# Kernel optimization log

Measured on AMD Instinct MI355X. Metric: run time of the kernel, lower is better.

## Reference

```python
import jax, jax.numpy as jnp
import numpy as np

DIM = 64
HID = 64      # hidden_dim
BATCH = 16384


def setup_inputs() -> dict:
    key = jax.random.key(0)
    ks = jax.random.split(key, 11)
    s = 0.05
    x = jax.random.normal(ks[0], (BATCH, DIM), dtype=jnp.float32)
    # network 0: Linear(1,H) -> ReLU -> Linear(H,2)
    w0 = jax.random.normal(ks[1], (1, HID), dtype=jnp.float32) * s
    b0 = jax.random.normal(ks[2], (HID,), dtype=jnp.float32) * s
    v0 = jax.random.normal(ks[3], (HID, 2), dtype=jnp.float32) * s
    c0 = jax.random.normal(ks[4], (2,), dtype=jnp.float32) * s
    # networks 1..DIM-1: Linear(i,H) -> ReLU -> Linear(H,H) -> ReLU -> Linear(H,2)
    # first-layer weights padded to full width DIM; columns >= i are masked out in reference().
    W1 = jax.random.normal(ks[5], (DIM - 1, DIM, HID), dtype=jnp.float32) * s
    B1 = jax.random.normal(ks[6], (DIM - 1, HID), dtype=jnp.float32) * s
    W2 = jax.random.normal(ks[7], (DIM - 1, HID, HID), dtype=jnp.float32) * s
    B2 = jax.random.normal(ks[8], (DIM - 1, HID), dtype=jnp.float32) * s
    W3 = jax.random.normal(ks[9], (DIM - 1, HID, 2), dtype=jnp.float32) * s
    B3 = jax.random.normal(ks[10], (DIM - 1, 2), dtype=jnp.float32) * s
    return {"x": x, "w0": w0, "b0": b0, "v0": v0, "c0": c0,
            "W1": W1, "B1": B1, "W2": W2, "B2": B2, "W3": W3, "B3": B3}


def reference(x, w0, b0, v0, c0, W1, B1, W2, B2, W3, B3):
    B, dim = x.shape
    # mask[i, j] = 1 if j < (i+1): network i+1 sees x[:, :i+1] prefix of width i+1... actually width i+1? No:
    # network index k (k = 1..dim-1) sees x[:, :k]. Row i of the stacks corresponds to k = i+1,
    # so valid input columns are j < i+1.
    mask = (jnp.arange(dim)[None, :] <= jnpp_dummy) if False else (jnp.arange(dim)[None, :] < (jnp.arange(1, dim)[:, None]))
    mask = mask.astype(x.dtype)                      # [dim-1, dim]
    W1m = W1 * mask[:, :, None]                      # zero out padded input columns
    h1 = jax.nn.relu(jnp.einsum('bd,idh->bih', x, W1m) + B1)   # [B, dim-1, H]
    h2 = jax.nn.relu(jnp.einsum('bih,ihg->big', h1, W2) + B2)  # [B, dim-1, H]
    out = jnp.einsum('big,igo->bio', h2, W3) + B3               # [B, dim-1, 2]
    # network 0 receives a constant ones input -> output is constant across the batch
    h0 = jax.nn.relu(w0[0] + b0)                     # [H]
    out0 = h0 @ v0 + c0                              # [2]
    out0 = jnp.broadcast_to(out0[None, None, :], (B, 1, 2))
    full = jnp.concatenate([out0, out], axis=1)      # [B, dim, 2]
    scales = jnp.clip(full[..., 0], -5.0, 5.0)
    translations = full[..., 1]
    return scales, translations

jnp_dummy = None
```

## Files before the change

### kernel.cpp

```cpp
#include <hip/hip_runtime.h>
#include <hip/hip_bf16.h>

#define BATCH 16384

typedef __attribute__((ext_vector_type(8))) short short8;
typedef __attribute__((ext_vector_type(4))) short short4v;
typedef __attribute__((ext_vector_type(2))) short sshort2;
typedef __attribute__((ext_vector_type(8))) unsigned short ushort8;
typedef __attribute__((ext_vector_type(4))) unsigned short ushort4v;
typedef __attribute__((ext_vector_type(4))) float float4v;

#define FR_A1      0u
#define FR_A2      516096u
#define FR_A3      1032192u
#define FR_SIZE    1161216u
#define XBF_SIZE   2097152u

__device__ __forceinline__ unsigned int packbf2(float a, float b) {
#if __has_builtin(__builtin_amdgcn_cvt_pk_bf16_f32)
    typedef __attribute__((ext_vector_type(2))) __bf16 bf2_t;
    union { bf2_t h; unsigned int u; } v;
    v.h = __builtin_amdgcn_cvt_pk_bf16_f32(a, b);
    return v.u;
#else
    union { __hip_bfloat162 h; unsigned int u; } v;
    v.h = __float22bfloat162_rn(make_float2(a, b));
    return v.u;
#endif
}
__device__ __forceinline__ unsigned int relu_pk(unsigned int u) {
#if __has_builtin(__builtin_elementwise_max)
    union { sshort2 s; unsigned int w; } v; v.w = u;
    v.s = __builtin_elementwise_max(v.s, (sshort2)0);
    return v.w;
#else
    unsigned int lo = (u & 0x8000u) ? 0u : (u & 0xFFFFu);
    unsigned int hi = (u & 0x80000000u) ? 0u : (u & 0xFFFF0000u);
    return lo | hi;
#endif
}
__device__ __forceinline__ unsigned int cvt_relu(float a, float b) {
    return relu_pk(packbf2(a, b));
}
__device__ __forceinline__ unsigned short f2bf(float a) {
    union { __hip_bfloat16 h; unsigned short u; } v;
    v.h = __float2bfloat16(a);
    return v.u;
}

__global__ __launch_bounds__(256) void setup_kernel(
    const float* __restrict__ x,
    const float* __restrict__ W1,
    const float* __restrict__ W2,
    const float* __restrict__ W3,
    char* __restrict__ frag,
    char* __restrict__ xbf)
{
    const int b = blockIdx.x;
    const int t = threadIdx.x;

    if (b >= 63) {
        const int idx = (b - 63) * 256 + t;
        const float* xp = x + (size_t)idx * 16;
        char* dst = xbf + (size_t)idx * 32;
        #pragma unroll
        for (int h = 0; h < 2; ++h) {
            float4v f0 = *(const float4v*)(xp + h * 8);
            float4v f1 = *(const float4v*)(xp + h * 8 + 4);
            union { ushort8 s; unsigned int u[4]; } p;
            p.u[0] = packbf2(f0[0], f0[1]);
            p.u[1] = packbf2(f0[2], f0[3]);
            p.u[2] = packbf2(f1[0], f1[1]);
            p.u[3] = packbf2(f1[2], f1[3]);
            *(ushort8*)(dst + h * 16) = p.s;
        }
        return;
    }

    const int kn   = b;
    const int net  = kn + 1;
    const int lane = t & 63;
    const int grp  = t >> 6;
    const int lq   = lane & 15;
    const int quad = lane >> 4;

    {
        const int h = lq + 16 * grp;
        ushort8 a10, a11;
        #pragma unroll
        for (int j = 0; j < 8; ++j) {
            const int d0 = quad * 8 + j;
            const int d1 = d0 + 32;
            a10[j] = (d0 < net) ? f2bf(W1[kn * 4096 + d0 * 64 + h]) : (unsigned short)0;
            a11[j] = (d1 < net) ? f2bf(W1[kn * 4096 + d1 * 64 + h]) : (unsigned short)0;
        }
        char* dst = frag + FR_A1 + kn * 8192 + grp * 2048 + lane * 32;
        *(ushort8*)(dst)      = a10;
        *(ushort8*)(dst + 16) = a11;
    }

    {
        const int g = lq + 16 * grp;
        #pragma unroll
        for (int th = 0; th < 4; ++th) {
            ushort4v v;
            #pragma unroll
            for (int i = 0; i < 4; ++i) {
                const int h = quad * 4 + 16 * th + i;
                v[i] = f2bf(W2[kn * 4096 + h * 64 + g]);
            }
            *(ushort4v*)(frag + FR_A2 + kn * 8192 + lane * 128 + grp * 32 + th * 8) = v;
        }
    }

    {
        ushort4v v;
        #pragma unroll
        for (int i = 0; i < 4; ++i) {
            const int g = quad * 4 + 16 * grp + i;
            v[i] = (lq < 2) ? f2bf(W3[kn * 128 + g * 2 + lq]) : (unsigned short)0;
        }
        *(ushort4v*)(frag + FR_A3 + kn * 2048 + lane * 32 + grp * 8) = v;
    }
}

template <bool XBF>
__global__ __launch_bounds__(256, 3) void arnet_main4(
    const float* __restrict__ x,
    const char* __restrict__ xbf,
    const char* __restrict__ frag,
    const float* __restrict__ w0, const float* __restrict__ b0,
    const float* __restrict__ v0, const float* __restrict__ c0,
    const float* __restrict__ B1, const float* __restrict__ B2,
    const float* __restrict__ B3,
    float* __restrict__ out)
{
    const int bi    = blockIdx.x;
    const int chunk = bi & 63;
    const int g     = bi >> 6;
    const int t     = threadIdx.x;

    const int lane = t & 63;
    const int w    = t >> 6;
    const int lq   = lane & 15;
    const int quad = lane >> 4;

    __shared__ float sOut[2][256][5];

    const int rowbase = chunk * 256 + w * 64;

    short8 xf[4][2];
    #pragma unroll
    for (int tm = 0; tm < 4; ++tm) {
        if (XBF) {
            const char* base = xbf + (size_t)(rowbase + 16 * tm + lq) * 128 + quad * 16;
            xf[tm][0] = *(const short8*)(base);
            xf[tm][1] = *(const short8*)(base + 64);
        } else {
            const float* xr = x + (size_t)(rowbase + 16 * tm + lq) * 64 + quad * 8;
            #pragma unroll
            for (int half = 0; half < 2; ++half) {
                float4v f0 = *(const float4v*)(xr + 32 * half);
                float4v f1 = *(const float4v*)(xr + 32 * half + 4);
                union { short8 s; unsigned int u[4]; } p;
                p.u[0] = packbf2(f0[0], f0[1]);
                p.u[1] = packbf2(f0[2], f0[3]);
                p.u[2] = packbf2(f1[0], f1[1]);
                p.u[3] = packbf2(f1[2], f1[3]);
                xf[tm][half] = p.s;
            }
        }
    }

    #pragma unroll 1
    for (int idx = 0; idx < 4; ++idx) {
        const int net = g * 4 + idx;

        if (net == 0) {
            float s = 0.f, tr = 0.f;
            #pragma unroll 8
            for (int j = 0; j < 64; ++j) {
                float h = fmaxf(w0[j] + b0[j], 0.f);
                s  += h * v0[2 * j];
                tr += h * v0[2 * j + 1];
            }
            s += c0[0];
            tr += c0[1];
            s = fminf(fmaxf(s, -5.f), 5.f);
            sOut[0][t][0] = s;
            sOut[1][t][0] = tr;
            continue;
        }

        const int kn = net - 1;
        const char* pA1 = frag + FR_A1 + kn * 8192 + lane * 32;
        const char* pA2 = frag + FR_A2 + kn * 8192 + lane * 128;
        const char* pA3 = frag + FR_A3 + kn * 2048 + lane * 32;

        float4v acc2[4][4];
        #pragma unroll
        for (int th = 0; th < 4; ++th) {
            short8 a10 = *(const short8*)(pA1 + th * 2048);
            short8 a11 = *(const short8*)(pA1 + th * 2048 + 16);
            float4v bias1 = *(const float4v*)(B1 + kn * 64 + quad * 4 + 16 * th);
            short4v bf1[4];
            #pragma unroll
            for (int tm = 0; tm < 4; ++tm) {
                float4v acc1;
                acc1 = __builtin_amdgcn_mfma_f32_16x16x32_bf16(a10, xf[tm][0], bias1, 0, 0, 0);
                acc1 = __builtin_amdgcn_mfma_f32_16x16x32_bf16(a11, xf[tm][1], acc1, 0, 0, 0);
                union { short4v s; unsigned int u[2]; } pk;
                pk.u[0] = cvt_relu(acc1[0], acc1[1]);
                pk.u[1] = cvt_relu(acc1[2], acc1[3]);
                bf1[tm] = pk.s;
            }
            if (th == 0) {
                #pragma unroll
                for (int tg = 0; tg < 4; ++tg) {
                    short4v a2 = *(const short4v*)(pA2 + tg * 32);
                    float4v bias2 = *(const float4v*)(B2 + kn * 64 + quad * 4 + 16 * tg);
                    #pragma unroll
                    for (int tm = 0; tm < 4; ++tm)
                        acc2[tg][tm] = __builtin_amdgcn_mfma_f32_16x16x16bf16_1k(a2, bf1[tm], bias2, 0, 0, 0);
                }
            } else {
                #pragma unroll
                for (int tg = 0; tg < 4; ++tg) {
                    short4v a2 = *(const short4v*)(pA2 + tg * 32 + th * 8);
                    #pragma unroll
                    for (int tm = 0; tm < 4; ++tm)
                        acc2[tg][tm] = __builtin_amdgcn_mfma_f32_16x16x16bf16_1k(a2, bf1[tm], acc2[tg][tm], 0, 0, 0);
                }
            }
        }

        float4v c3v;
        c3v[0] = B3[kn * 2]; c3v[1] = B3[kn * 2 + 1]; c3v[2] = 0.f; c3v[3] = 0.f;
        float4v acc3[4];
        #pragma unroll
        for (int tg = 0; tg < 4; ++tg) {
            short4v a3 = *(const short4v*)(pA3 + tg * 8);
            #pragma unroll
            for (int tm = 0; tm < 4; ++tm) {
                union { short4v s; unsigned int u[2]; } pk;
                pk.u[0] = cvt_relu(acc2[tg][tm][0], acc2[tg][tm][1]);
                pk.u[1] = cvt_relu(acc2[tg][tm][2], acc2[tg][tm][3]);
                acc3[tm] = __builtin_amdgcn_mfma_f32_16x16x16bf16_1k(a3, pk.s, (tg == 0) ? c3v : acc3[tm], 0, 0, 0);
            }
        }

        if (quad == 0) {
            #pragma unroll
            for (int tm = 0; tm < 4; ++tm) {
                const int lr = w * 64 + 16 * tm + lq;
                sOut[0][lr][idx] = fminf(fmaxf(acc3[tm][0], -5.f), 5.f);
                sOut[1][lr][idx] = acc3[tm][1];
            }
        }
    }

    __syncthreads();

    {
        const int row = t;
        const size_t grow = (size_t)chunk * 256 + row;
        #pragma unroll
        for (int o = 0; o < 2; ++o) {
            float4v v4;
            #pragma unroll
            for (int j = 0; j < 4; ++j) v4[j] = sOut[o][row][j];
            float* dst = out + ((size_t)o * BATCH + grow) * 64 + 4 * g;
            *(float4v*)(dst) = v4;
        }
    }
}

#define WPAD 72
__global__ __launch_bounds__(256) void arnet_fallback(
    const float* __restrict__ x, const float* __restrict__ w0, const float* __restrict__ b0,
    const float* __restrict__ v0, const float* __restrict__ c0,
    const float* __restrict__ W1, const float* __restrict__ B1,
    const float* __restrict__ W2, const float* __restrict__ B2,
    const float* __restrict__ W3, const float* __restrict__ B3,
    float* __restrict__ out)
{
    const int bi = blockIdx.x;
    const int net = bi >> 5;
    const int tile = bi & 31;
    const int t = threadIdx.x;
    if (net == 0) {
        float s = 0.f, tr = 0.f;
        for (int j = 0; j < 64; ++j) {
            float h = fmaxf(w0[j] + b0[j], 0.f);
            s += h * v0[2 * j]; tr += h * v0[2 * j + 1];
        }
        s += c0[0]; tr += c0[1];
        s = fminf(fmaxf(s, -5.f), 5.f);
        const size_t r0 = (size_t)tile * 512;
        out[(r0 + t) * 64] = s; out[(size_t)BATCH * 64 + (r0 + t) * 64] = tr;
        out[(r0 + 256 + t) * 64] = s; out[(size_t)BATCH * 64 + (r0 + 256 + t) * 64] = tr;
        return;
    }
    __shared__ unsigned short sW1T[64 * WPAD];
    __shared__ unsigned short sW2T[64 * WPAD];
    __shared__ unsigned short sW3T[2 * 64];
    __shared__ float sB1[64];
    __shared__ float sB2[64];
    const int kn = net - 1;
    {
        const int hb = (t & 15) * 4, jb = (t >> 4) * 4;
        const float* src1 = W1 + kn * 4096;
        const float* src2 = W2 + kn * 4096;
        float4v a[4], b[4];
        for (int jj = 0; jj < 4; ++jj) {
            a[jj] = *(const float4v*)(src1 + (jb + jj) * 64 + hb);
            if (jb + jj >= net) a[jj] = (float4v)0.f;
            b[jj] = *(const float4v*)(src2 + (jb + jj) * 64 + hb);
        }
        for (int hh = 0; hh < 4; ++hh) {
            ushort4v ra, rb;
            for (int jj = 0; jj < 4; ++jj) { ra[jj] = f2bf(a[jj][hh]); rb[jj] = f2bf(b[jj][hh]); }
            *(ushort4v*)(&sW1T[(hb + hh) * WPAD + jb]) = ra;
            *(ushort4v*)(&sW2T[(hb + hh) * WPAD + jb]) = rb;
        }
    }
    if (t < 64) {
        sW3T[t] = f2bf(W3[kn * 128 + t * 2]);
        sW3T[64 + t] = f2bf(W3[kn * 128 + t * 2 + 1]);
        sB1[t] = B1[kn * 64 + t];
        sB2[t] = B2[kn * 64 + t];
    }
    const float b30 = B3[kn * 2], b31 = B3[kn * 2 + 1];
    __syncthreads();
    const int lane = t & 63, w = t >> 6, lq = lane & 15, quad = lane >> 4;
    for (int pass = 0; pass < 2; ++pass) {
        const int rowbase = tile * 512 + pass * 256 + w * 64;
        short8 xf[4][2];
        for (int tm = 0; tm < 4; ++tm) {
            const float* xr = x + (size_t)(rowbase + 16 * tm + lq) * 64 + quad * 8;
            for (int half = 0; half < 2; ++half) {
                float4v f0 = *(const float4v*)(xr + 32 * half);
                float4v f1 = *(const float4v*)(xr + 32 * half + 4);
                union { short8 s; unsigned int u[4]; } p;
                p.u[0] = packbf2(f0[0], f0[1]); p.u[1] = packbf2(f0[2], f0[3]);
                p.u[2] = packbf2(f1[0], f1[1]); p.u[3] = packbf2(f1[2], f1[3]);
                xf[tm][half] = p.s;
            }
        }
        float4v acc2[4][4];
        for (int tg = 0; tg < 4; ++tg) {
            float4v bias2 = *(const float4v*)(&sB2[quad * 4 + 16 * tg]);
            for (int tm = 0; tm < 4; ++tm) acc2[tg][tm] = bias2;
        }
        for (int th = 0; th < 4; ++th) {
            float4v bias1 = *(const float4v*)(&sB1[quad * 4 + 16 * th]);
            short8 a10 = *(const short8*)(&sW1T[(lq + 16 * th) * WPAD + quad * 8]);
            short8 a11 = *(const short8*)(&sW1T[(lq + 16 * th) * WPAD + quad * 8 + 32]);
            float4v acc1[4];
            for (int tm = 0; tm < 4; ++tm) {
                acc1[tm] = bias1;
                acc1[tm] = __builtin_amdgcn_mfma_f32_16x16x32_bf16(a10, xf[tm][0], acc1[tm], 0, 0, 0);
                acc1[tm] = __builtin_amdgcn_mfma_f32_16x16x32_bf16(a11, xf[tm][1], acc1[tm], 0, 0, 0);
            }
            short4v bf1[4];
            for (int tm = 0; tm < 4; ++tm) {
                union { short4v s; unsigned int u[2]; } pk;
                pk.u[0] = cvt_relu(acc1[tm][0], acc1[tm][1]);
                pk.u[1] = cvt_relu(acc1[tm][2], acc1[tm][3]);
                bf1[tm] = pk.s;
            }
            for (int tg = 0; tg < 4; ++tg) {
                short4v a2 = *(const short4v*)(&sW2T[(lq + 16 * tg) * WPAD + quad * 4 + 16 * th]);
                for (int tm = 0; tm < 4; ++tm)
                    acc2[tg][tm] = __builtin_amdgcn_mfma_f32_16x16x16bf16_1k(a2, bf1[tm], acc2[tg][tm], 0, 0, 0);
            }
        }
        float4v acc3[4];
        for (int tm = 0; tm < 4; ++tm) { acc3[tm][0] = b30; acc3[tm][1] = b31; acc3[tm][2] = 0.f; acc3[tm][3] = 0.f; }
        for (int tg = 0; tg < 4; ++tg) {
            short4v a3 = (short4v)0;
            if (lq < 2) a3 = *(const short4v*)(&sW3T[lq * 64 + quad * 4 + 16 * tg]);
            for (int tm = 0; tm < 4; ++tm) {
                union { short4v s; unsigned int u[2]; } pk;
                pk.u[0] = cvt_relu(acc2[tg][tm][0], acc2[tg][tm][1]);
                pk.u[1] = cvt_relu(acc2[tg][tm][2], acc2[tg][tm][3]);
                acc3[tm] = __builtin_amdgcn_mfma_f32_16x16x16bf16_1k(a3, pk.s, acc3[tm], 0, 0, 0);
            }
        }
        if (quad == 0) {
            for (int tm = 0; tm < 4; ++tm) {
                const size_t r = (size_t)(rowbase + 16 * tm + lq);
                out[r * 64 + net] = fminf(fmaxf(acc3[tm][0], -5.f), 5.f);
                out[(size_t)BATCH * 64 + r * 64 + net] = acc3[tm][1];
            }
        }
    }
}

extern "C" void kernel_launch(void* const* d_in, const int* in_sizes, int n_in,
                              void* d_out, int out_size, void* d_ws, size_t ws_size,
                              hipStream_t stream) {
    const float* x  = (const float*)d_in[0];
    const float* w0 = (const float*)d_in[1];
    const float* b0 = (const float*)d_in[2];
    const float* v0 = (const float*)d_in[3];
    const float* c0 = (const float*)d_in[4];
    const float* W1 = (const float*)d_in[5];
    const float* B1 = (const float*)d_in[6];
    const float* W2 = (const float*)d_in[7];
    const float* B2 = (const float*)d_in[8];
    const float* W3 = (const float*)d_in[9];
    const float* B3 = (const float*)d_in[10];
    float* out = (float*)d_out;
    char* ws = (char*)d_ws;

    const dim3 blk(256);

    if (ws_size >= FR_SIZE + XBF_SIZE) {
        char* xbf = ws + FR_SIZE;
        setup_kernel<<<dim3(63 + 256), blk, 0, stream>>>(x, W1, W2, W3, ws, xbf);
        arnet_main4<true><<<dim3(1024), blk, 0, stream>>>(
            x, xbf, ws, w0, b0, v0, c0, B1, B2, B3, out);
    } else if (ws_size >= FR_SIZE) {
        setup_kernel<<<dim3(63), blk, 0, stream>>>(x, W1, W2, W3, ws, nullptr);
        arnet_main4<false><<<dim3(1024), blk, 0, stream>>>(
            x, nullptr, ws, w0, b0, v0, c0, B1, B2, B3, out);
    } else {
        arnet_fallback<<<dim3(64 * 32), blk, 0, stream>>>(
            x, w0, b0, v0, c0, W1, B1, W2, B2, W3, B3, out);
    }
}
```

Before: 120.2 us.

## Process two networks per iteration and eight per block to interleave MFMA chains

Each block now evaluates eight networks instead of four, processed in interleaved pairs. Each pair runs two independent MFMA dependency chains side by side to raise instruction-level parallelism, and the bf16 x fragments loaded into registers are reused across twice as many networks. The grid is halved to 512 blocks and the launch bound lowered to 2 blocks per CU so roughly twice the accumulator registers fit. The trade-off is fewer resident waves per CU, plus one redundant evaluation of network 1 in the pair that contains the constant network 0.

```diff
diff --git a/kernel.cpp b/kernel.cpp
--- a/kernel.cpp
+++ b/kernel.cpp
@@ -125,7 +125,7 @@
 }
 
 template <bool XBF>
-__global__ __launch_bounds__(256, 3) void arnet_main4(
+__global__ __launch_bounds__(256, 2) void arnet_main5(
     const float* __restrict__ x,
     const char* __restrict__ xbf,
     const char* __restrict__ frag,
@@ -145,7 +145,7 @@
     const int lq   = lane & 15;
     const int quad = lane >> 4;
 
-    __shared__ float sOut[2][256][5];
+    __shared__ float sOut[2][256][9];
 
     const int rowbase = chunk * 256 + w * 64;
 
@@ -173,10 +173,12 @@
     }
 
     #pragma unroll 1
-    for (int idx = 0; idx < 4; ++idx) {
-        const int net = g * 4 + idx;
-
-        if (net == 0) {
+    for (int pair = 0; pair < 4; ++pair) {
+        int na = g * 8 + 2 * pair;
+        int nb = na + 1;
+        int ca = 2 * pair, cb = 2 * pair + 1;
+
+        if (na == 0) {
             float s = 0.f, tr = 0.f;
             #pragma unroll 8
             for (int j = 0; j < 64; ++j) {
@@ -189,63 +191,86 @@
             s = fminf(fmaxf(s, -5.f), 5.f);
             sOut[0][t][0] = s;
             sOut[1][t][0] = tr;
-            continue;
-        }
-
-        const int kn = net - 1;
-        const char* pA1 = frag + FR_A1 + kn * 8192 + lane * 32;
-        const char* pA2 = frag + FR_A2 + kn * 8192 + lane * 128;
-        const char* pA3 = frag + FR_A3 + kn * 2048 + lane * 32;
-
-        float4v acc2[4][4];
+            na = 1; ca = 1;
+        }
+
+        const int ka = na - 1, kb = nb - 1;
+        const char* pA1a = frag + FR_A1 + ka * 8192 + lane * 32;
+        const char* pA2a = frag + FR_A2 + ka * 8192 + lane * 128;
+        const char* pA3a = frag + FR_A3 + ka * 2048 + lane * 32;
+        const char* pA1b = frag + FR_A1 + kb * 8192 + lane * 32;
+        const char* pA2b = frag + FR_A2 + kb * 8192 + lane * 128;
+        const char* pA3b = frag + FR_A3 + kb * 2048 + lane * 32;
+
+        float4v acc2a[4][4], acc2b[4][4];
         #pragma unroll
         for (int th = 0; th < 4; ++th) {
-            short8 a10 = *(const short8*)(pA1 + th * 2048);
-            short8 a11 = *(const short8*)(pA1 + th * 2048 + 16);
-            float4v bias1 = *(const float4v*)(B1 + kn * 64 + quad * 4 + 16 * th);
-            short4v bf1[4];
-            #pragma unroll
-            for (int tm = 0; tm < 4; ++tm) {
-                float4v acc1;
-                acc1 = __builtin_amdgcn_mfma_f32_16x16x32_bf16(a10, xf[tm][0], bias1, 0, 0, 0);
-                acc1 = __builtin_amdgcn_mfma_f32_16x16x32_bf16(a11, xf[tm][1], acc1, 0, 0, 0);
-                union { short4v s; unsigned int u[2]; } pk;
-                pk.u[0] = cvt_relu(acc1[0], acc1[1]);
-                pk.u[1] = cvt_relu(acc1[2], acc1[3]);
-                bf1[tm] = pk.s;
+            short8 a10a = *(const short8*)(pA1a + th * 2048);
+            short8 a11a = *(const short8*)(pA1a + th * 2048 + 16);
+            short8 a10b = *(const short8*)(pA1b + th * 2048);
+            short8 a11b = *(const short8*)(pA1b + th * 2048 + 16);
+            float4v bias1a = *(const float4v*)(B1 + ka * 64 + quad * 4 + 16 * th);
+            float4v bias1b = *(const float4v*)(B1 + kb * 64 + quad * 4 + 16 * th);
+            short4v bf1a[4], bf1b[4];
+            #pragma unroll
+            for (int tm = 0; tm < 4; ++tm) {
+                float4v acc1a, acc1b;
+                acc1a = __builtin_amdgcn_mfma_f32_16x16x32_bf16(a10a, xf[tm][0], bias1a, 0, 0, 0);
+                acc1b = __builtin_amdgcn_mfma_f32_16x16x32_bf16(a10b, xf[tm][0], bias1b, 0, 0, 0);
+                acc1a = __builtin_amdgcn_mfma_f32_16x16x32_bf16(a11a, xf[tm][1], acc1a, 0, 0, 0);
+                acc1b = __builtin_amdgcn_mfma_f32_16x16x32_bf16(a11b, xf[tm][1], acc1b, 0, 0, 0);
+                union { short4v s; unsigned int u[2]; } pka, pkb;
+                pka.u[0] = cvt_relu(acc1a[0], acc1a[1]);
+                pka.u[1] = cvt_relu(acc1a[2], acc1a[3]);
+                pkb.u[0] = cvt_relu(acc1b[0], acc1b[1]);
+                pkb.u[1] = cvt_relu(acc1b[2], acc1b[3]);
+                bf1a[tm] = pka.s;
+                bf1b[tm] = pkb.s;
             }
             if (th == 0) {
                 #pragma unroll
                 for (int tg = 0; tg < 4; ++tg) {
-                    short4v a2 = *(const short4v*)(pA2 + tg * 32);
-                    float4v bias2 = *(const float4v*)(B2 + kn * 64 + quad * 4 + 16 * tg);
+                    short4v a2a = *(const short4v*)(pA2a + tg * 32);
+                    short4v a2b = *(const short4v*)(pA2b + tg * 32);
+                    float4v bias2a = *(const float4v*)(B2 + ka * 64 + quad * 4 + 16 * tg);
+                    float4v bias2b = *(const float4v*)(B2 + kb * 64 + quad * 4 + 16 * tg);
                     #pragma unroll
-                    for (int tm = 0; tm < 4; ++tm)
-                        acc2[tg][tm] = __builtin_amdgcn_mfma_f32_16x16x16bf16_1k(a2, bf1[tm], bias2, 0, 0, 0);
+                    for (int tm = 0; tm < 4; ++tm) {
+                        acc2a[tg][tm] = __builtin_amdgcn_mfma_f32_16x16x16bf16_1k(a2a, bf1a[tm], bias2a, 0, 0, 0);
+                        acc2b[tg][tm] = __builtin_amdgcn_mfma_f32_16x16x16bf16_1k(a2b, bf1b[tm], bias2b, 0, 0, 0);
+                    }
                 }
             } else {
                 #pragma unroll
                 for (int tg = 0; tg < 4; ++tg) {
-                    short4v a2 = *(const short4v*)(pA2 + tg * 32 + th * 8);
+                    short4v a2a = *(const short4v*)(pA2a + tg * 32 + th * 8);
+                    short4v a2b = *(const short4v*)(pA2b + tg * 32 + th * 8);
                     #pragma unroll
-                    for (int tm = 0; tm < 4; ++tm)
-                        acc2[tg][tm] = __builtin_amdgcn_mfma_f32_16x16x16bf16_1k(a2, bf1[tm], acc2[tg][tm], 0, 0, 0);
+                    for (int tm = 0; tm < 4; ++tm) {
+                        acc2a[tg][tm] = __builtin_amdgcn_mfma_f32_16x16x16bf16_1k(a2a, bf1a[tm], acc2a[tg][tm], 0, 0, 0);
+                        acc2b[tg][tm] = __builtin_amdgcn_mfma_f32_16x16x16bf16_1k(a2b, bf1b[tm], acc2b[tg][tm], 0, 0, 0);
+                    }
                 }
             }
         }
 
-        float4v c3v;
-        c3v[0] = B3[kn * 2]; c3v[1] = B3[kn * 2 + 1]; c3v[2] = 0.f; c3v[3] = 0.f;
-        float4v acc3[4];
+        float4v c3a, c3b;
+        c3a[0] = B3[ka * 2]; c3a[1] = B3[ka * 2 + 1]; c3a[2] = 0.f; c3a[3] = 0.f;
+        c3b[0] = B3[kb * 2]; c3b[1] = B3[kb * 2 + 1]; c3b[2] = 0.f; c3b[3] = 0.f;
+        float4v acc3a[4], acc3b[4];
         #pragma unroll
         for (int tg = 0; tg < 4; ++tg) {
-            short4v a3 = *(const short4v*)(pA3 + tg * 8);
-            #pragma unroll
-            for (int tm = 0; tm < 4; ++tm) {
-                union { short4v s; unsigned int u[2]; } pk;
-                pk.u[0] = cvt_relu(acc2[tg][tm][0], acc2[tg][tm][1]);
-                pk.u[1] = cvt_relu(acc2[tg][tm][2], acc2[tg][tm][3]);
-                acc3[tm] = __builtin_amdgcn_mfma_f32_16x16x16bf16_1k(a3, pk.s, (tg == 0) ? c3v : acc3[tm], 0, 0, 0);
+            short4v a3a = *(const short4v*)(pA3a + tg * 8);
+            short4v a3b = *(const short4v*)(pA3b + tg * 8);
+            #pragma unroll
+            for (int tm = 0; tm < 4; ++tm) {
+                union { short4v s; unsigned int u[2]; } pka, pkb;
+                pka.u[0] = cvt_relu(acc2a[tg][tm][0], acc2a[tg][tm][1]);
+                pka.u[1] = cvt_relu(acc2a[tg][tm][2], acc2a[tg][tm][3]);
+                pkb.u[0] = cvt_relu(acc2b[tg][tm][0], acc2b[tg][tm][1]);
+                pkb.u[1] = cvt_relu(acc2b[tg][tm][2], acc2b[tg][tm][3]);
+                acc3a[tm] = __builtin_amdgcn_mfma_f32_16x16x16bf16_1k(a3a, pka.s, (tg == 0) ? c3a : acc3a[tm], 0, 0, 0);
+                acc3b[tm] = __builtin_amdgcn_mfma_f32_16x16x16bf16_1k(a3b, pkb.s, (tg == 0) ? c3b : acc3b[tm], 0, 0, 0);
             }
         }
 
@@ -253,8 +278,10 @@
             #pragma unroll
             for (int tm = 0; tm < 4; ++tm) {
                 const int lr = w * 64 + 16 * tm + lq;
-                sOut[0][lr][idx] = fminf(fmaxf(acc3[tm][0], -5.f), 5.f);
-                sOut[1][lr][idx] = acc3[tm][1];
+                sOut[0][lr][ca] = fminf(fmaxf(acc3a[tm][0], -5.f), 5.f);
+                sOut[1][lr][ca] = acc3a[tm][1];
+                sOut[0][lr][cb] = fminf(fmaxf(acc3b[tm][0], -5.f), 5.f);
+                sOut[1][lr][cb] = acc3b[tm][1];
             }
         }
     }
@@ -266,11 +293,12 @@
         const size_t grow = (size_t)chunk * 256 + row;
         #pragma unroll
         for (int o = 0; o < 2; ++o) {
-            float4v v4;
-            #pragma unroll
-            for (int j = 0; j < 4; ++j) v4[j] = sOut[o][row][j];
-            float* dst = out + ((size_t)o * BATCH + grow) * 64 + 4 * g;
-            *(float4v*)(dst) = v4;
+            float4v va, vb;
+            #pragma unroll
+            for (int j = 0; j < 4; ++j) { va[j] = sOut[o][row][j]; vb[j] = sOut[o][row][4 + j]; }
+            float* dst = out + ((size_t)o * BATCH + grow) * 64 + 8 * g;
+            *(float4v*)(dst)     = va;
+            *(float4v*)(dst + 4) = vb;
         }
     }
 }
@@ -419,11 +447,11 @@
     if (ws_size >= FR_SIZE + XBF_SIZE) {
         char* xbf = ws + FR_SIZE;
         setup_kernel<<<dim3(63 + 256), blk, 0, stream>>>(x, W1, W2, W3, ws, xbf);
-        arnet_main4<true><<<dim3(1024), blk, 0, stream>>>(
+        arnet_main5<true><<<dim3(512), blk, 0, stream>>>(
             x, xbf, ws, w0, b0, v0, c0, B1, B2, B3, out);
     } else if (ws_size >= FR_SIZE) {
         setup_kernel<<<dim3(63), blk, 0, stream>>>(x, W1, W2, W3, ws, nullptr);
-        arnet_main4<false><<<dim3(1024), blk, 0, stream>>>(
+        arnet_main5<false><<<dim3(512), blk, 0, stream>>>(
             x, nullptr, ws, w0, b0, v0, c0, B1, B2, B3, out);
     } else {
         arnet_fallback<<<dim3(64 * 32), blk, 0, stream>>>(
```

After: 122.4 us. No clear change (+1.9%).
